# Optimization experiments

Hardware: AMD Instinct MI355X
Metric: run time of the kernel (lower is better)

## Reference

```python
import jax, jax.numpy as jnp
import numpy as np

CUTOFF = 5.0
N_GAUSS = 32
N_HEADS = 8
MAX_Z = 100


def _gather(feat, idx):
    # feat: (B, N, ...), idx: (B, N, K) -> (B, N, K, ...)
    return jax.vmap(lambda f, i: f[i])(feat, idx)


def setup_inputs() -> dict:
    key = jax.random.key(0)
    ks = jax.random.split(key, 10)
    B, N, K, D, G = 16, 512, 48, 128, N_GAUSS
    s = 0.05
    positions = jax.random.normal(ks[0], (B, N, 3), dtype=jnp.float32) * 2.0
    z = jax.random.randint(ks[1], (B, N), 0, MAX_Z)
    neighbors = jax.random.randint(ks[2], (B, N, K), 0, N)
    neighbor_mask = jnp.ones((B, N, K), dtype=jnp.float32)
    embedding = jax.random.normal(ks[3], (MAX_Z, D), jnp.float32)
    embedding = embedding.at[0].set(0.0)  # padding_idx=0
    filt_W = jax.random.normal(ks[4], (G, D), jnp.float32) * s
    filt_b = jnp.zeros((D,), jnp.float32)
    Wq = jax.random.normal(ks[5], (D, D), jnp.float32) * s
    Wk = jax.random.normal(ks[6], (D, D), jnp.float32) * s
    Wv = jax.random.normal(ks[7], (D, D), jnp.float32) * s
    Wo = jax.random.normal(ks[8], (D, D), jnp.float32) * s
    return dict(positions=positions, z=z, neighbors=neighbors,
                neighbor_mask=neighbor_mask, embedding=embedding,
                filt_W=filt_W, filt_b=filt_b, Wq=Wq, Wk=Wk, Wv=Wv, Wo=Wo)


def reference(positions, z, neighbors, neighbor_mask, embedding,
              filt_W, filt_b, Wq, Wk, Wv, Wo):
    B, N, K = neighbors.shape
    D = embedding.shape[1]
    H = N_HEADS
    hd = D // H

    # atom embeddings
    x = embedding[z]                                        # (B, N, D)

    # AtomDistances: neighbor gather + distances
    pos_j = _gather(positions, neighbors)                   # (B, N, K, 3)
    r_vec = pos_j - positions[:, :, None, :]
    r_ij = jnp.sqrt(jnp.sum(r_vec * r_vec, axis=-1) + 1e-12)  # (B, N, K)

    # Positional_Embedding: prepend self-distance 0.01, log-normal smearing
    r_iij = jnp.concatenate(
        [jnp.full((B, N, 1), 0.01, r_ij.dtype), r_ij], axis=-1)  # (B, N, K+1)
    offsets = jnp.linspace(np.log(0.1), np.log(CUTOFF), N_GAUSS).astype(r_ij.dtype)
    width = offsets[1] - offsets[0]
    coeff = -0.5 / (width * width)
    f_iij = jnp.exp(coeff * (jnp.log(r_iij)[..., None] - offsets) ** 2)  # (B,N,K+1,G)

    # filter network + cosine cutoff
    W = f_iij @ filt_W + filt_b                             # (B, N, K+1, D)
    C = 0.5 * (jnp.cos(r_iij * jnp.pi / CUTOFF) + 1.0) * (r_iij < CUTOFF)
    W = W * C[..., None]

    # gather neighbor embeddings, include self (ego) node
    x_j = _gather(x, neighbors)                             # (B, N, K, D)
    nodes = jnp.concatenate([x[:, :, None, :], x_j], axis=2)  # (B, N, K+1, D)
    kv_in = nodes * W

    # EgoAttention: center atom attends over {self + neighbors}
    q = (x @ Wq).reshape(B, N, H, hd)
    k = (kv_in @ Wk).reshape(B, N, K + 1, H, hd)
    v = (kv_in @ Wv).reshape(B, N, K + 1, H, hd)
    scores = jnp.einsum('bnhd,bnkhd->bnhk', q, k) / jnp.sqrt(jnp.float32(hd))
    mask = jnp.concatenate(
        [jnp.ones((B, N, 1), neighbor_mask.dtype), neighbor_mask], axis=-1)
    scores = jnp.where(mask[:, :, None, :] > 0, scores, jnp.float32(-1e9))
    attn = jax.nn.softmax(scores, axis=-1)
    agg = jnp.einsum('bnhk,bnkhd->bnhd', attn, v).reshape(B, N, D)
    v_msg = agg @ Wo

    # residual update (apply_transition_function=False): x = x + v
    return x + v_msg
```

## Files before the change

kernel.cpp:

```cpp
#include <hip/hip_runtime.h>
#include <math.h>

#define NTHREADS 256

typedef _Float16 v8h __attribute__((ext_vector_type(8)));
typedef float    v4f __attribute__((ext_vector_type(4)));

namespace {
constexpr int D   = 128;
constexpr int H   = 8;
constexpr int KNB = 48;
constexpr int KP1 = 49;
constexpr int NN  = 512;

constexpr size_t WS_P    = 0;
constexpr size_t WS_QKZ  = 16777216;
constexpr size_t WS_WVOT = 16982016;
constexpr size_t WS_QZ   = 17244160;
constexpr size_t WS_FWTP = 17295360;
constexpr size_t WS_NEED = 17303552;

constexpr float LOG_LO = -2.302585092994046f;
constexpr float LOG_HI =  1.609437912434100f;
constexpr float GWIDTH = (LOG_HI - LOG_LO) / 31.0f;
constexpr float GCOEFF = -0.5f / (GWIDTH * GWIDTH);
constexpr float PI_OVER_CUT = 3.14159265358979323846f / 5.0f;
}

union H8U4 { _Float16 h[8]; uint4 u; };

__global__ __launch_bounds__(NTHREADS) void k0a_qz(
    const float* __restrict__ embedding, const float* __restrict__ Wq,
    float* __restrict__ qz) {
  const int idx = blockIdx.x * NTHREADS + threadIdx.x;
  const int zz = idx >> 7, j = idx & 127;
  float a0 = 0.f, a1 = 0.f, a2 = 0.f, a3 = 0.f;
  for (int e = 0; e < 128; e += 4) {
    a0 = fmaf(embedding[zz * 128 + e + 0], Wq[(e + 0) * 128 + j], a0);
    a1 = fmaf(embedding[zz * 128 + e + 1], Wq[(e + 1) * 128 + j], a1);
    a2 = fmaf(embedding[zz * 128 + e + 2], Wq[(e + 2) * 128 + j], a2);
    a3 = fmaf(embedding[zz * 128 + e + 3], Wq[(e + 3) * 128 + j], a3);
  }
  qz[idx] = (a0 + a1) + (a2 + a3);
}

__global__ __launch_bounds__(NTHREADS) void k0b_prep(
    const float* __restrict__ filt_W, const float* __restrict__ Wk,
    const float* __restrict__ Wv, const float* __restrict__ Wo,
    const float* __restrict__ qz, _Float16* __restrict__ QKz,
    _Float16* __restrict__ WvoT, _Float16* __restrict__ fWTP) {
  const int blk = blockIdx.x;
  const int tid = threadIdx.x;
  if (blk < 400) {
    const int idx = blk * NTHREADS + tid;
    const int zz = idx >> 10, hc = idx & 1023, h = hc >> 7, c = hc & 127;
    float acc = 0.0f;
#pragma unroll
    for (int e = 0; e < 16; ++e)
      acc = fmaf(qz[zz * 128 + h * 16 + e], Wk[c * 128 + h * 16 + e], acc);
    QKz[idx] = (_Float16)(acc * 0.25f);
  } else if (blk < 912) {
    const int idx = (blk - 400) * NTHREADS + tid;
    const int cp = idx >> 10, hd = idx & 1023, h = hd >> 7, d = hd & 127;
    float acc = 0.0f;
#pragma unroll
    for (int cc = 0; cc < 16; ++cc)
      acc = fmaf(Wv[d * 128 + h * 16 + cc], Wo[(h * 16 + cc) * 128 + cp], acc);
    WvoT[idx] = (_Float16)acc;
  } else {
    const int i = (blk - 912) * NTHREADS + tid;
    const int nt = i >> 6, quad = (i >> 4) & 3, col = i & 15;
    H8U4 pk;
#pragma unroll
    for (int j = 0; j < 8; ++j)
      pk.h[j] = (_Float16)filt_W[(quad * 8 + j) * 128 + nt * 16 + col];
    *(uint4*)&fWTP[i * 8] = pk.u;
  }
}

namespace k2c {
constexpr int KV_S  = 136;
constexpr int QK_S  = 136;
constexpr int ATH_S = 72;
constexpr int SC_S  = 52;
constexpr int OFF_KV  = 0;
constexpr int OFF_QK  = 13328;
constexpr int OFF_ATH = 15504;
constexpr int OFF_SC  = 16800;
constexpr int OFF_LR  = 18464;
constexpr int OFF_C   = 18672;
constexpr int OFF_MSK = 18880;
constexpr int OFF_ZJ  = 19088;
constexpr int SMEM    = 19296;
}

__global__ __launch_bounds__(NTHREADS, 8) void k2_attn(
    const float* __restrict__ positions, const int* __restrict__ z,
    const int* __restrict__ neighbors, const float* __restrict__ nmask,
    const float* __restrict__ embedding, const float* __restrict__ filt_b,
    const _Float16* __restrict__ fWTP, const _Float16* __restrict__ QKz,
    _Float16* __restrict__ P) {
  using namespace k2c;
  __shared__ __align__(16) char smem[SMEM];
  _Float16* s_kv  = reinterpret_cast<_Float16*>(smem + OFF_KV);
  _Float16* s_qk  = reinterpret_cast<_Float16*>(smem + OFF_QK);
  _Float16* s_ath = reinterpret_cast<_Float16*>(smem + OFF_ATH);
  float*    s_sc  = reinterpret_cast<float*>(smem + OFF_SC);
  float*    s_lr  = reinterpret_cast<float*>(smem + OFF_LR);
  float*    s_C   = reinterpret_cast<float*>(smem + OFF_C);
  float*    s_msk = reinterpret_cast<float*>(smem + OFF_MSK);
  int*      s_zj  = reinterpret_cast<int*>(smem + OFF_ZJ);

  const int a   = blockIdx.x;
  const int b   = a >> 9;
  const int n   = a & (NN - 1);
  const int tid = threadIdx.x;
  const int w    = tid >> 6;
  const int lane = tid & 63;
  const int col  = lane & 15;
  const int quad = lane >> 4;

  const int zc = __builtin_amdgcn_readfirstlane(z[a]);

  if (tid < KP1) {
    int j; float m;
    if (tid == 0) { j = n; m = 1.0f; }
    else { j = neighbors[a * KNB + tid - 1]; m = nmask[a * KNB + tid - 1]; }
    float r;
    if (tid == 0) r = 0.01f;
    else {
      const float dx = positions[(b * NN + j) * 3 + 0] - positions[a * 3 + 0];
      const float dy = positions[(b * NN + j) * 3 + 1] - positions[a * 3 + 1];
      const float dz = positions[(b * NN + j) * 3 + 2] - positions[a * 3 + 2];
      r = sqrtf(dx * dx + dy * dy + dz * dz + 1e-12f);
    }
    s_lr[tid]  = __logf(r);
    s_C[tid]   = (r < 5.0f) ? (0.5f * (__cosf(r * PI_OVER_CUT) + 1.0f)) : 0.0f;
    s_msk[tid] = m;
    s_zj[tid]  = z[b * NN + j];
  } else if (tid >= 128) {
    const int i = tid - 128;
    const uint4 v = *(const uint4*)(QKz + (size_t)zc * 1024 + i * 8);
    const int h = i >> 4, dd = (i & 15) * 8;
    *(uint4*)&s_qk[h * QK_S + dd] = v;
  }
  __syncthreads();

  {
    const int trow = 16 * w + col;
    const float lr = s_lr[trow < KP1 ? trow : KP1 - 1];
    v8h afrag;
#pragma unroll
    for (int j = 0; j < 8; ++j) {
      const int g = quad * 8 + j;
      const float dlt = lr - (LOG_LO + (float)g * GWIDTH);
      afrag[j] = (_Float16)__expf(GCOEFF * dlt * dlt);
    }
    v4f acc[8];
#pragma unroll
    for (int nt = 0; nt < 8; ++nt) {
      const v8h bfrag = *(const v8h*)(fWTP + (((nt * 4 + quad) * 16 + col) * 8));
      v4f zero = {0.0f, 0.0f, 0.0f, 0.0f};
      acc[nt] = __builtin_amdgcn_mfma_f32_16x16x32_f16(afrag, bfrag, zero, 0, 0, 0);
    }
    float bv[8];
#pragma unroll
    for (int nt = 0; nt < 8; ++nt) bv[nt] = filt_b[nt * 16 + col];
#pragma unroll
    for (int reg = 0; reg < 4; ++reg) {
      const int t = 16 * w + quad * 4 + reg;
      const bool valid = t < KP1;
      const float cf = valid ? s_C[t] : 0.0f;
      const int   zj = s_zj[valid ? t : KP1 - 1];
      const float* erow = embedding + (size_t)zj * D;
#pragma unroll
      for (int nt = 0; nt < 8; ++nt) {
        const int c = nt * 16 + col;
        if (valid)
          s_kv[t * KV_S + c] = (_Float16)((acc[nt][reg] + bv[nt]) * cf * erow[c]);
      }
    }
  }
  __syncthreads();

  {
    v4f sacc = {0.0f, 0.0f, 0.0f, 0.0f};
#pragma unroll
    for (int ks = 0; ks < 4; ++ks) {
      const v8h afr = *(const v8h*)&s_kv[(16 * w + col) * KV_S + ks * 32 + quad * 8];
      const v8h bfr = *(const v8h*)&s_qk[col * QK_S + ks * 32 + quad * 8];
      sacc = __builtin_amdgcn_mfma_f32_16x16x32_f16(afr, bfr, sacc, 0, 0, 0);
    }
    const int h = col;
    if (h < H) {
#pragma unroll
      for (int reg = 0; reg < 4; ++reg) {
        const int t = 16 * w + quad * 4 + reg;
        if (t < KP1) {
          float sc = sacc[reg];
          if (s_msk[t] <= 0.0f) sc = -1e9f;
          s_sc[h * SC_S + t] = sc;
        }
      }
    }
  }
  __syncthreads();

  if (tid < 64) {
    const int h  = tid >> 3;
    const int sl = tid & 7;
    float* row = &s_sc[h * SC_S];
    float m = -1e30f;
    for (int t = sl; t < KP1; t += 8) m = fmaxf(m, row[t]);
    m = fmaxf(m, __shfl_xor(m, 1));
    m = fmaxf(m, __shfl_xor(m, 2));
    m = fmaxf(m, __shfl_xor(m, 4));
    float s = 0.0f;
    float ev[7];
#pragma unroll
    for (int i = 0; i < 7; ++i) {
      const int t = sl + i * 8;
      const float e = (t < KP1) ? __expf(row[t] - m) : 0.0f;
      ev[i] = e;
      s += e;
    }
    s += __shfl_xor(s, 1);
    s += __shfl_xor(s, 2);
    s += __shfl_xor(s, 4);
    const float inv = 1.0f / s;
#pragma unroll
    for (int i = 0; i < 7; ++i) {
      const int t = sl + i * 8;
      if (t < KP1) s_ath[h * ATH_S + t] = (_Float16)(ev[i] * inv);
    }
  } else if (tid < 128) {
    const int i = tid - 64;
    for (int idx = i; idx < 8 * 15; idx += 64) {
      const int h = idx / 15;
      const int t = KP1 + idx % 15;
      s_ath[h * ATH_S + t] = (_Float16)0.0f;
    }
  }
  __syncthreads();

  {
    const int arow = (col < 8) ? col : 8;
    const v8h a0 = *(const v8h*)&s_ath[arow * ATH_S + quad * 8];
    const v8h a1 = *(const v8h*)&s_ath[arow * ATH_S + 32 + quad * 8];
#pragma unroll
    for (int nti = 0; nti < 2; ++nti) {
      const int c = (2 * w + nti) * 16 + col;
      v8h b0, b1;
#pragma unroll
      for (int j = 0; j < 8; ++j) {
        b0[j] = s_kv[(quad * 8 + j) * KV_S + c];
        const int t1 = 32 + quad * 8 + j;
        const _Float16 vv = s_kv[t1 * KV_S + c];
        b1[j] = (t1 < KP1) ? vv : (_Float16)0.0f;
      }
      v4f pacc = {0.0f, 0.0f, 0.0f, 0.0f};
      pacc = __builtin_amdgcn_mfma_f32_16x16x32_f16(a0, b0, pacc, 0, 0, 0);
      pacc = __builtin_amdgcn_mfma_f32_16x16x32_f16(a1, b1, pacc, 0, 0, 0);
      if (quad < 2) {
#pragma unroll
        for (int reg = 0; reg < 4; ++reg) {
          const int h = quad * 4 + reg;
          P[(size_t)a * 1024 + h * 128 + c] = (_Float16)pacc[reg];
        }
      }
    }
  }
}

__global__ __launch_bounds__(NTHREADS) void k3_gemm(
    const int* __restrict__ z, const float* __restrict__ embedding,
    const _Float16* __restrict__ P, const _Float16* __restrict__ WvoT,
    float* __restrict__ out) {
  __shared__ __align__(16) _Float16 sA[16 * 136];
  __shared__ __align__(16) _Float16 sB[128 * 136];
  __shared__ int s_z[16];
  const int a0  = blockIdx.x * 16;
  const int tid = threadIdx.x;
  const int w    = tid >> 6;
  const int lane = tid & 63;
  const int col  = lane & 15;
  const int quad = lane >> 4;
  if (tid < 16) s_z[tid] = z[a0 + tid];

  v4f acc[2];
  acc[0] = (v4f){0.f, 0.f, 0.f, 0.f};
  acc[1] = (v4f){0.f, 0.f, 0.f, 0.f};

  for (int kc = 0; kc < 8; ++kc) {
    const int k0 = kc * 128;
    __syncthreads();
    {
      const int ai = tid >> 4, sl = tid & 15;
      *(uint4*)&sA[ai * 136 + sl * 8] =
          *(const uint4*)(P + (size_t)(a0 + ai) * 1024 + k0 + sl * 8);
    }
#pragma unroll
    for (int it = 0; it < 8; ++it) {
      const int idx = it * NTHREADS + tid;
      const int cp = idx >> 4, sl = idx & 15;
      *(uint4*)&sB[cp * 136 + sl * 8] =
          *(const uint4*)(WvoT + (size_t)cp * 1024 + k0 + sl * 8);
    }
    __syncthreads();
#pragma unroll
    for (int ks = 0; ks < 4; ++ks) {
      const v8h af  = *(const v8h*)&sA[col * 136 + ks * 32 + quad * 8];
      const v8h bf0 = *(const v8h*)&sB[(w * 32 + col)      * 136 + ks * 32 + quad * 8];
      const v8h bf1 = *(const v8h*)&sB[(w * 32 + 16 + col) * 136 + ks * 32 + quad * 8];
      acc[0] = __builtin_amdgcn_mfma_f32_16x16x32_f16(af, bf0, acc[0], 0, 0, 0);
      acc[1] = __builtin_amdgcn_mfma_f32_16x16x32_f16(af, bf1, acc[1], 0, 0, 0);
    }
  }
#pragma unroll
  for (int reg = 0; reg < 4; ++reg) {
    const int al = quad * 4 + reg;
    const float* xr = embedding + (size_t)s_z[al] * 128;
#pragma unroll
    for (int nt = 0; nt < 2; ++nt) {
      const int cp = w * 32 + nt * 16 + col;
      out[(size_t)(a0 + al) * 128 + cp] = xr[cp] + acc[nt][reg];
    }
  }
}

namespace mono {
constexpr int KV_S = 136, QK_S = 136, FWT_S = 40, ATH_S = 64, SC_S = 52, P_S = 132;
constexpr int OFF_KV = 0, OFF_FWT = 17408, OFF_P = 17408, OFF_AGG = 21632,
              OFF_QK = 27648, OFF_ATH = 32000, OFF_SC = 34048, OFF_Q = 35712,
              OFF_LR = 36224, OFF_C = 36432, OFF_MSK = 36640, OFF_ZJ = 36848,
              SMEM = 37056;
}

__global__ __launch_bounds__(NTHREADS, 4) void tdt_mono(
    const float* __restrict__ positions, const int* __restrict__ z,
    const int* __restrict__ neighbors, const float* __restrict__ nmask,
    const float* __restrict__ embedding, const float* __restrict__ filt_W,
    const float* __restrict__ filt_b, const float* __restrict__ Wq,
    const float* __restrict__ Wk, const float* __restrict__ Wv,
    const float* __restrict__ Wo, float* __restrict__ out) {
  using namespace mono;
  __shared__ __align__(16) char smem[SMEM];
  _Float16* s_kvh = reinterpret_cast<_Float16*>(smem + OFF_KV);
  _Float16* s_fWT = reinterpret_cast<_Float16*>(smem + OFF_FWT);
  float*    s_p   = reinterpret_cast<float*>(smem + OFF_P);
  float*    s_agg = reinterpret_cast<float*>(smem + OFF_AGG);
  _Float16* s_qkh = reinterpret_cast<_Float16*>(smem + OFF_QK);
  _Float16* s_ath = reinterpret_cast<_Float16*>(smem + OFF_ATH);
  float*    s_sc  = reinterpret_cast<float*>(smem + OFF_SC);
  float*    s_q   = reinterpret_cast<float*>(smem + OFF_Q);
  float*    s_lr  = reinterpret_cast<float*>(smem + OFF_LR);
  float*    s_C   = reinterpret_cast<float*>(smem + OFF_C);
  float*    s_msk = reinterpret_cast<float*>(smem + OFF_MSK);
  int*      s_zj  = reinterpret_cast<int*>(smem + OFF_ZJ);
  const int a = blockIdx.x, b = a >> 9, n = a & (NN - 1), tid = threadIdx.x;
  const int w = tid >> 6, lane = tid & 63, col = lane & 15, quad = lane >> 4;
  const int zc = __builtin_amdgcn_readfirstlane(z[a]);
  if (tid < KP1) {
    int j; float m;
    if (tid == 0) { j = n; m = 1.0f; }
    else { j = neighbors[a * KNB + tid - 1]; m = nmask[a * KNB + tid - 1]; }
    float r;
    if (tid == 0) r = 0.01f;
    else {
      const float dx = positions[(b * NN + j) * 3 + 0] - positions[a * 3 + 0];
      const float dy = positions[(b * NN + j) * 3 + 1] - positions[a * 3 + 1];
      const float dz = positions[(b * NN + j) * 3 + 2] - positions[a * 3 + 2];
      r = sqrtf(dx * dx + dy * dy + dz * dz + 1e-12f);
    }
    s_lr[tid] = __logf(r);
    s_C[tid] = (r < 5.0f) ? (0.5f * (__cosf(r * PI_OVER_CUT) + 1.0f)) : 0.0f;
    s_msk[tid] = m;
    s_zj[tid] = z[b * NN + j];
  } else if (tid >= 64 && tid < 128) {
    const int i = tid - 64;
    for (int rep = 0; rep < 64; ++rep) {
      const int idx = rep * 64 + i;
      const int g = idx >> 7, c = idx & 127;
      s_fWT[c * FWT_S + g] = (_Float16)filt_W[idx];
    }
    unsigned* kz = reinterpret_cast<unsigned*>(s_kvh);
    for (int d0 = KP1 * (KV_S / 2) + i; d0 < 64 * (KV_S / 2); d0 += 64) kz[d0] = 0u;
  } else if (tid >= 128) {
    const int d = tid - 128;
    float acc = 0.0f;
    for (int e = 0; e < D; e += 4) {
      const float x0 = embedding[zc * D + e + 0];
      const float x1 = embedding[zc * D + e + 1];
      const float x2 = embedding[zc * D + e + 2];
      const float x3 = embedding[zc * D + e + 3];
      acc = fmaf(x0, Wq[(e + 0) * D + d], acc);
      acc = fmaf(x1, Wq[(e + 1) * D + d], acc);
      acc = fmaf(x2, Wq[(e + 2) * D + d], acc);
      acc = fmaf(x3, Wq[(e + 3) * D + d], acc);
    }
    s_q[d] = acc;
  }
  __syncthreads();
  {
    const int trow = 16 * w + col;
    const float lr = s_lr[trow < KP1 ? trow : KP1 - 1];
    v8h afrag;
#pragma unroll
    for (int j = 0; j < 8; ++j) {
      const int g = quad * 8 + j;
      const float dlt = lr - (LOG_LO + (float)g * GWIDTH);
      afrag[j] = (_Float16)__expf(GCOEFF * dlt * dlt);
    }
    v4f acc[8];
#pragma unroll
    for (int nt = 0; nt < 8; ++nt) {
      const v8h bfrag = *(const v8h*)&s_fWT[(nt * 16 + col) * FWT_S + quad * 8];
      v4f zero = {0.0f, 0.0f, 0.0f, 0.0f};
      acc[nt] = __builtin_amdgcn_mfma_f32_16x16x32_f16(afrag, bfrag, zero, 0, 0, 0);
    }
    float bv[8];
#pragma unroll
    for (int nt = 0; nt < 8; ++nt) bv[nt] = filt_b[nt * 16 + col];
#pragma unroll
    for (int reg = 0; reg < 4; ++reg) {
      const int t = 16 * w + quad * 4 + reg;
      const bool valid = t < KP1;
      float cf = 0.0f; int zj = 0;
      if (valid) { cf = s_C[t]; zj = s_zj[t]; }
      const float* erow = embedding + (size_t)zj * D;
#pragma unroll
      for (int nt = 0; nt < 8; ++nt) {
        const int c = nt * 16 + col;
        if (valid)
          s_kvh[t * KV_S + c] = (_Float16)((acc[nt][reg] + bv[nt]) * cf * erow[c]);
      }
    }
  }
  {
    const int h = tid & 7;
    const float4 q0 = *(const float4*)&s_q[h * 16 + 0];
    const float4 q1 = *(const float4*)&s_q[h * 16 + 4];
    const float4 q2 = *(const float4*)&s_q[h * 16 + 8];
    const float4 q3 = *(const float4*)&s_q[h * 16 + 12];
#pragma unroll
    for (int it = 0; it < 4; ++it) {
      const int d = ((it * NTHREADS + tid) >> 3);
      const float* wk = &Wk[d * D + h * 16];
      const float4 w0 = *(const float4*)&wk[0];
      const float4 w1 = *(const float4*)&wk[4];
      const float4 w2 = *(const float4*)&wk[8];
      const float4 w3 = *(const float4*)&wk[12];
      float s = w0.x * q0.x;
      s = fmaf(w0.y, q0.y, s); s = fmaf(w0.z, q0.z, s); s = fmaf(w0.w, q0.w, s);
      s = fmaf(w1.x, q1.x, s); s = fmaf(w1.y, q1.y, s);
      s = fmaf(w1.z, q1.z, s); s = fmaf(w1.w, q1.w, s);
      s = fmaf(w2.x, q2.x, s); s = fmaf(w2.y, q2.y, s);
      s = fmaf(w2.z, q2.z, s); s = fmaf(w2.w, q2.w, s);
      s = fmaf(w3.x, q3.x, s); s = fmaf(w3.y, q3.y, s);
      s = fmaf(w3.z, q3.z, s); s = fmaf(w3.w, q3.w, s);
      s_qkh[h * QK_S + d] = (_Float16)s;
    }
  }
  __syncthreads();
  {
    v4f sacc = {0.0f, 0.0f, 0.0f, 0.0f};
#pragma unroll
    for (int ks = 0; ks < 4; ++ks) {
      const v8h afr = *(const v8h*)&s_kvh[(16 * w + col) * KV_S + ks * 32 + quad * 8];
      const v8h bfr = *(const v8h*)&s_qkh[col * QK_S + ks * 32 + quad * 8];
      sacc = __builtin_amdgcn_mfma_f32_16x16x32_f16(afr, bfr, sacc, 0, 0, 0);
    }
    const int h = col;
    if (h < H) {
#pragma unroll
      for (int reg = 0; reg < 4; ++reg) {
        const int t = 16 * w + quad * 4 + reg;
        if (t < KP1) {
          float sc = sacc[reg] * 0.25f;
          if (s_msk[t] <= 0.0f) sc = -1e9f;
          s_sc[h * SC_S + t] = sc;
        }
      }
    }
  }
  __syncthreads();
  if (tid < 64) {
    const int h = tid >> 3, sl = tid & 7;
    float* row = &s_sc[h * SC_S];
    float m = -1e30f;
    for (int t = sl; t < KP1; t += 8) m = fmaxf(m, row[t]);
    m = fmaxf(m, __shfl_xor(m, 1));
    m = fmaxf(m, __shfl_xor(m, 2));
    m = fmaxf(m, __shfl_xor(m, 4));
    float s = 0.0f;
    float ev[7];
#pragma unroll
    for (int i = 0; i < 7; ++i) {
      const int t = sl + i * 8;
      const float e = (t < KP1) ? __expf(row[t] - m) : 0.0f;
      ev[i] = e; s += e;
    }
    s += __shfl_xor(s, 1);
    s += __shfl_xor(s, 2);
    s += __shfl_xor(s, 4);
    const float inv = 1.0f / s;
#pragma unroll
    for (int i = 0; i < 7; ++i) {
      const int t = sl + i * 8;
      if (t < KP1) s_ath[h * ATH_S + t] = (_Float16)(ev[i] * inv);
    }
  } else if (tid < 128) {
    const int i = tid - 64;
    for (int idx = i; idx < 8 * 15; idx += 64) {
      const int h = idx / 15, t = KP1 + idx % 15;
      s_ath[h * ATH_S + t] = (_Float16)0.0f;
    }
  }
  __syncthreads();
  {
    const v8h a0 = *(const v8h*)&s_ath[col * ATH_S + quad * 8];
    const v8h a1 = *(const v8h*)&s_ath[col * ATH_S + 32 + quad * 8];
#pragma unroll
    for (int nti = 0; nti < 2; ++nti) {
      const int c = (2 * w + nti) * 16 + col;
      v8h b0, b1;
#pragma unroll
      for (int j = 0; j < 8; ++j) {
        b0[j] = s_kvh[(quad * 8 + j) * KV_S + c];
        b1[j] = s_kvh[(32 + quad * 8 + j) * KV_S + c];
      }
      v4f pacc = {0.0f, 0.0f, 0.0f, 0.0f};
      pacc = __builtin_amdgcn_mfma_f32_16x16x32_f16(a0, b0, pacc, 0, 0, 0);
      pacc = __builtin_amdgcn_mfma_f32_16x16x32_f16(a1, b1, pacc, 0, 0, 0);
#pragma unroll
      for (int reg = 0; reg < 4; ++reg) {
        const int h = quad * 4 + reg;
        if (h < H) s_p[h * P_S + c] = pacc[reg];
      }
    }
  }
  __syncthreads();
  if (tid < 128) {
    const int c = tid;
    const float* pr = &s_p[(c >> 4) * P_S];
    float acc = 0.0f;
    for (int d = 0; d < D; d += 4) {
      const float4 p4 = *(const float4*)&pr[d];
      acc = fmaf(p4.x, Wv[(d + 0) * D + c], acc);
      acc = fmaf(p4.y, Wv[(d + 1) * D + c], acc);
      acc = fmaf(p4.z, Wv[(d + 2) * D + c], acc);
      acc = fmaf(p4.w, Wv[(d + 3) * D + c], acc);
    }
    s_agg[c] = acc;
  }
  __syncthreads();
  if (tid < 128) {
    const int c = tid;
    float acc = embedding[zc * D + c];
    for (int e = 0; e < D; e += 4) {
      const float4 g4 = *(const float4*)&s_agg[e];
      acc = fmaf(g4.x, Wo[(e + 0) * D + c], acc);
      acc = fmaf(g4.y, Wo[(e + 1) * D + c], acc);
      acc = fmaf(g4.z, Wo[(e + 2) * D + c], acc);
      acc = fmaf(g4.w, Wo[(e + 3) * D + c], acc);
    }
    out[a * D + c] = acc;
  }
}

extern "C" void kernel_launch(void* const* d_in, const int* in_sizes, int n_in,
                              void* d_out, int out_size, void* d_ws, size_t ws_size,
                              hipStream_t stream) {
  const float* positions = (const float*)d_in[0];
  const int*   z         = (const int*)d_in[1];
  const int*   neighbors = (const int*)d_in[2];
  const float* nmask     = (const float*)d_in[3];
  const float* embedding = (const float*)d_in[4];
  const float* filt_W    = (const float*)d_in[5];
  const float* filt_b    = (const float*)d_in[6];
  const float* Wq        = (const float*)d_in[7];
  const float* Wk        = (const float*)d_in[8];
  const float* Wv        = (const float*)d_in[9];
  const float* Wo        = (const float*)d_in[10];
  float* out = (float*)d_out;
  const int natoms = in_sizes[1];

  if (ws_size >= WS_NEED) {
    char* ws = (char*)d_ws;
    _Float16* P    = (_Float16*)(ws + WS_P);
    _Float16* QKz  = (_Float16*)(ws + WS_QKZ);
    _Float16* WvoT = (_Float16*)(ws + WS_WVOT);
    float*    qz   = (float*)(ws + WS_QZ);
    _Float16* fWTP = (_Float16*)(ws + WS_FWTP);
    k0a_qz<<<50, NTHREADS, 0, stream>>>(embedding, Wq, qz);
    k0b_prep<<<914, NTHREADS, 0, stream>>>(filt_W, Wk, Wv, Wo, qz, QKz, WvoT, fWTP);
    k2_attn<<<natoms, NTHREADS, 0, stream>>>(positions, z, neighbors, nmask,
                                             embedding, filt_b, fWTP, QKz, P);
    k3_gemm<<<natoms / 16, NTHREADS, 0, stream>>>(z, embedding, P, WvoT, out);
  } else {
    tdt_mono<<<natoms, NTHREADS, 0, stream>>>(positions, z, neighbors, nmask,
                                              embedding, filt_W, filt_b,
                                              Wq, Wk, Wv, Wo, out);
  }
}
```

Measured before the change: 130.4 us.

## Use fp16 embedding table, vectorize P stores, split output GEMM columns

Result: no change. 131.5 us (+0.9%).

```diff
diff --git a/kernel.cpp b/kernel.cpp
--- a/kernel.cpp
+++ b/kernel.cpp
@@ -18,7 +18,8 @@
 constexpr size_t WS_WVOT = 16982016;
 constexpr size_t WS_QZ   = 17244160;
 constexpr size_t WS_FWTP = 17295360;
-constexpr size_t WS_NEED = 17303552;
+constexpr size_t WS_EMBH = 17303552;
+constexpr size_t WS_NEED = 17329152;
 
 constexpr float LOG_LO = -2.302585092994046f;
 constexpr float LOG_HI =  1.609437912434100f;
@@ -28,6 +29,7 @@
 }
 
 union H8U4 { _Float16 h[8]; uint4 u; };
+union H4U2 { _Float16 h[4]; uint2 u; };
 
 __global__ __launch_bounds__(NTHREADS) void k0a_qz(
     const float* __restrict__ embedding, const float* __restrict__ Wq,
@@ -47,8 +49,9 @@
 __global__ __launch_bounds__(NTHREADS) void k0b_prep(
     const float* __restrict__ filt_W, const float* __restrict__ Wk,
     const float* __restrict__ Wv, const float* __restrict__ Wo,
-    const float* __restrict__ qz, _Float16* __restrict__ QKz,
-    _Float16* __restrict__ WvoT, _Float16* __restrict__ fWTP) {
+    const float* __restrict__ qz, const float* __restrict__ embedding,
+    _Float16* __restrict__ QKz, _Float16* __restrict__ WvoT,
+    _Float16* __restrict__ fWTP, _Float16* __restrict__ embh) {
   const int blk = blockIdx.x;
   const int tid = threadIdx.x;
   if (blk < 400) {
@@ -61,13 +64,13 @@
     QKz[idx] = (_Float16)(acc * 0.25f);
   } else if (blk < 912) {
     const int idx = (blk - 400) * NTHREADS + tid;
-    const int cp = idx >> 10, hd = idx & 1023, h = hd >> 7, d = hd & 127;
+    const int cp = idx >> 10, kk = idx & 1023, d = kk >> 3, h = kk & 7;
     float acc = 0.0f;
 #pragma unroll
     for (int cc = 0; cc < 16; ++cc)
       acc = fmaf(Wv[d * 128 + h * 16 + cc], Wo[(h * 16 + cc) * 128 + cp], acc);
     WvoT[idx] = (_Float16)acc;
-  } else {
+  } else if (blk < 914) {
     const int i = (blk - 912) * NTHREADS + tid;
     const int nt = i >> 6, quad = (i >> 4) & 3, col = i & 15;
     H8U4 pk;
@@ -75,6 +78,9 @@
     for (int j = 0; j < 8; ++j)
       pk.h[j] = (_Float16)filt_W[(quad * 8 + j) * 128 + nt * 16 + col];
     *(uint4*)&fWTP[i * 8] = pk.u;
+  } else {
+    const int idx = (blk - 914) * NTHREADS + tid;
+    embh[idx] = (_Float16)embedding[idx];
   }
 }
 
@@ -97,7 +103,7 @@
 __global__ __launch_bounds__(NTHREADS, 8) void k2_attn(
     const float* __restrict__ positions, const int* __restrict__ z,
     const int* __restrict__ neighbors, const float* __restrict__ nmask,
-    const float* __restrict__ embedding, const float* __restrict__ filt_b,
+    const _Float16* __restrict__ embh, const float* __restrict__ filt_b,
     const _Float16* __restrict__ fWTP, const _Float16* __restrict__ QKz,
     _Float16* __restrict__ P) {
   using namespace k2c;
@@ -172,12 +178,13 @@
       const bool valid = t < KP1;
       const float cf = valid ? s_C[t] : 0.0f;
       const int   zj = s_zj[valid ? t : KP1 - 1];
-      const float* erow = embedding + (size_t)zj * D;
+      const _Float16* erow = embh + (size_t)zj * D;
 #pragma unroll
       for (int nt = 0; nt < 8; ++nt) {
         const int c = nt * 16 + col;
         if (valid)
-          s_kv[t * KV_S + c] = (_Float16)((acc[nt][reg] + bv[nt]) * cf * erow[c]);
+          s_kv[t * KV_S + c] =
+              (_Float16)((acc[nt][reg] + bv[nt]) * cf * (float)erow[c]);
       }
     }
   }
@@ -262,11 +269,10 @@
       pacc = __builtin_amdgcn_mfma_f32_16x16x32_f16(a0, b0, pacc, 0, 0, 0);
       pacc = __builtin_amdgcn_mfma_f32_16x16x32_f16(a1, b1, pacc, 0, 0, 0);
       if (quad < 2) {
-#pragma unroll
-        for (int reg = 0; reg < 4; ++reg) {
-          const int h = quad * 4 + reg;
-          P[(size_t)a * 1024 + h * 128 + c] = (_Float16)pacc[reg];
-        }
+        H4U2 pk;
+#pragma unroll
+        for (int reg = 0; reg < 4; ++reg) pk.h[reg] = (_Float16)pacc[reg];
+        *(uint2*)(P + (size_t)a * 1024 + c * 8 + quad * 4) = pk.u;
       }
     }
   }
@@ -277,9 +283,10 @@
     const _Float16* __restrict__ P, const _Float16* __restrict__ WvoT,
     float* __restrict__ out) {
   __shared__ __align__(16) _Float16 sA[16 * 136];
-  __shared__ __align__(16) _Float16 sB[128 * 136];
+  __shared__ __align__(16) _Float16 sB[64 * 136];
   __shared__ int s_z[16];
-  const int a0  = blockIdx.x * 16;
+  const int a0 = (blockIdx.x >> 1) * 16;
+  const int n0 = (blockIdx.x & 1) * 64;
   const int tid = threadIdx.x;
   const int w    = tid >> 6;
   const int lane = tid & 63;
@@ -287,9 +294,7 @@
   const int quad = lane >> 4;
   if (tid < 16) s_z[tid] = z[a0 + tid];
 
-  v4f acc[2];
-  acc[0] = (v4f){0.f, 0.f, 0.f, 0.f};
-  acc[1] = (v4f){0.f, 0.f, 0.f, 0.f};
+  v4f acc = (v4f){0.f, 0.f, 0.f, 0.f};
 
   for (int kc = 0; kc < 8; ++kc) {
     const int k0 = kc * 128;
@@ -300,31 +305,26 @@
           *(const uint4*)(P + (size_t)(a0 + ai) * 1024 + k0 + sl * 8);
     }
 #pragma unroll
-    for (int it = 0; it < 8; ++it) {
+    for (int it = 0; it < 4; ++it) {
       const int idx = it * NTHREADS + tid;
       const int cp = idx >> 4, sl = idx & 15;
       *(uint4*)&sB[cp * 136 + sl * 8] =
-          *(const uint4*)(WvoT + (size_t)cp * 1024 + k0 + sl * 8);
+          *(const uint4*)(WvoT + (size_t)(n0 + cp) * 1024 + k0 + sl * 8);
     }
     __syncthreads();
 #pragma unroll
     for (int ks = 0; ks < 4; ++ks) {
-      const v8h af  = *(const v8h*)&sA[col * 136 + ks * 32 + quad * 8];
-      const v8h bf0 = *(const v8h*)&sB[(w * 32 + col)      * 136 + ks * 32 + quad * 8];
-      const v8h bf1 = *(const v8h*)&sB[(w * 32 + 16 + col) * 136 + ks * 32 + quad * 8];
-      acc[0] = __builtin_amdgcn_mfma_f32_16x16x32_f16(af, bf0, acc[0], 0, 0, 0);
-      acc[1] = __builtin_amdgcn_mfma_f32_16x16x32_f16(af, bf1, acc[1], 0, 0, 0);
+      const v8h af = *(const v8h*)&sA[col * 136 + ks * 32 + quad * 8];
+      const v8h bf = *(const v8h*)&sB[(w * 16 + col) * 136 + ks * 32 + quad * 8];
+      acc = __builtin_amdgcn_mfma_f32_16x16x32_f16(af, bf, acc, 0, 0, 0);
     }
   }
 #pragma unroll
   for (int reg = 0; reg < 4; ++reg) {
     const int al = quad * 4 + reg;
-    const float* xr = embedding + (size_t)s_z[al] * 128;
-#pragma unroll
-    for (int nt = 0; nt < 2; ++nt) {
-      const int cp = w * 32 + nt * 16 + col;
-      out[(size_t)(a0 + al) * 128 + cp] = xr[cp] + acc[nt][reg];
-    }
+    const int cp = n0 + w * 16 + col;
+    out[(size_t)(a0 + al) * 128 + cp] =
+        embedding[(size_t)s_z[al] * 128 + cp] + acc[reg];
   }
 }
 
@@ -592,11 +592,13 @@
     _Float16* WvoT = (_Float16*)(ws + WS_WVOT);
     float*    qz   = (float*)(ws + WS_QZ);
     _Float16* fWTP = (_Float16*)(ws + WS_FWTP);
+    _Float16* embh = (_Float16*)(ws + WS_EMBH);
     k0a_qz<<<50, NTHREADS, 0, stream>>>(embedding, Wq, qz);
-    k0b_prep<<<914, NTHREADS, 0, stream>>>(filt_W, Wk, Wv, Wo, qz, QKz, WvoT, fWTP);
+    k0b_prep<<<964, NTHREADS, 0, stream>>>(filt_W, Wk, Wv, Wo, qz, embedding,
+                                           QKz, WvoT, fWTP, embh);
     k2_attn<<<natoms, NTHREADS, 0, stream>>>(positions, z, neighbors, nmask,
-                                             embedding, filt_b, fWTP, QKz, P);
-    k3_gemm<<<natoms / 16, NTHREADS, 0, stream>>>(z, embedding, P, WvoT, out);
+                                             embh, filt_b, fWTP, QKz, P);
+    k3_gemm<<<natoms / 16 * 2, NTHREADS, 0, stream>>>(z, embedding, P, WvoT, out);
   } else {
     tdt_mono<<<natoms, NTHREADS, 0, stream>>>(positions, z, neighbors, nmask,
                                               embedding, filt_W, filt_b,
```
